# Kernel tuning notes

Measured on AMD Instinct MI355X. Metric: run time of the kernel, lower is better.

The kernel has to match this reference:

```python
import jax, jax.numpy as jnp
import numpy as np

CH = 16      # channel_n
HID = 128    # hidden_n


def _max_pool3(a):
    # a: [B,1,H,W]; 3x3 max pool, stride 1, padding 1 (matches F.max_pool2d)
    return jax.lax.reduce_window(
        a, -jnp.inf, jax.lax.max,
        window_dimensions=(1, 1, 3, 3),
        window_strides=(1, 1, 1, 1),
        padding=((0, 0), (0, 0), (1, 1), (1, 1)))


def _living_mask(x):
    return _max_pool3(x[:, 3:4]) > 0.1


def _nca_step(x, perceive_w, w1, b1, w2, key):
    pre_life = _living_mask(x)                                  # [B,1,H,W] bool
    # depthwise sobel conv, identical weight layout/groups as torch Conv2d(groups=CH)
    p = jax.lax.conv_general_dilated(
        x, perceive_w, window_strides=(1, 1),
        padding=((1, 1), (1, 1)),
        dimension_numbers=('NCHW', 'OIHW', 'NCHW'),
        feature_group_count=CH)                                  # [B,2*CH,H,W]
    comb = jnp.transpose(jnp.concatenate([x, p], axis=1), (0, 2, 3, 1))  # [B,H,W,3*CH]
    h = jax.nn.relu(comb @ w1 + b1)                              # [B,H,W,HID]
    delta = jnp.transpose(h @ w2, (0, 3, 1, 2))                  # [B,CH,H,W]
    alpha = x[:, 3:4]
    upd = (jax.random.uniform(key, alpha.shape, dtype=x.dtype) < 0.5) & (alpha > 0.1)
    x = x + delta * upd.astype(x.dtype)
    life = pre_life & _living_mask(x)
    return x * life.astype(x.dtype)


def setup_inputs() -> dict:
    key = jax.random.key(0)
    kx, k1, k2 = jax.random.split(key, 3)
    B, H, W = 2, 128, 128
    x = jax.random.uniform(kx, (B, CH, H, W), dtype=jnp.float32)
    sobel_x = jnp.array([[-1., 0., 1.], [-2., 0., 2.], [-1., 0., 1.]], dtype=jnp.float32)
    sobel_y = jnp.array([[-1., -2., -1.], [0., 0., 0.], [1., 2., 1.]], dtype=jnp.float32)
    wx = jnp.tile(sobel_x[None, None], (CH, 1, 1, 1))
    wy = jnp.tile(sobel_y[None, None], (CH, 1, 1, 1))
    perceive_w = jnp.concatenate([wx, wy], axis=0)               # [2*CH,1,3,3]
    w1 = jax.random.normal(k1, (CH * 3, HID), dtype=jnp.float32) * 0.02
    b1 = jnp.zeros((HID,), dtype=jnp.float32)
    w2 = jax.random.normal(k2, (HID, CH), dtype=jnp.float32) * 0.02
    return {"x": x, "perceive_w": perceive_w, "w1": w1, "b1": b1, "w2": w2, "steps": 64}


def reference(x, perceive_w, w1, b1, w2, steps):
    keys = jax.random.split(jax.random.key(42), steps)

    def body(carry, k):
        return _nca_step(carry, perceive_w, w1, b1, w2, k), None

    x, _ = jax.lax.scan(body, x, keys)
    return x
```

## Files before the change

### kernel.cpp

```cpp
#include <hip/hip_runtime.h>
#include <stdint.h>

#define HH 128
#define WW 128
#define CHN 16
#define NPIX (HH*WW)
#define PLANE (CHN*NPIX)
#define STEPS 64
#define TW 8
#define TH 8

__host__ __device__ __forceinline__ uint32_t rotl32_(uint32_t x, int d) {
  return (x << d) | (x >> (32 - d));
}

__host__ __device__ __forceinline__ void tf2x32(uint32_t k0, uint32_t k1,
                                                uint32_t x0, uint32_t x1,
                                                uint32_t* o0, uint32_t* o1) {
  uint32_t ks0 = k0, ks1 = k1, ks2 = k0 ^ k1 ^ 0x1BD11BDAu;
  x0 += ks0; x1 += ks1;
  x0 += x1; x1 = rotl32_(x1, 13); x1 ^= x0;
  x0 += x1; x1 = rotl32_(x1, 15); x1 ^= x0;
  x0 += x1; x1 = rotl32_(x1, 26); x1 ^= x0;
  x0 += x1; x1 = rotl32_(x1, 6);  x1 ^= x0;
  x0 += ks1; x1 += ks2 + 1u;
  x0 += x1; x1 = rotl32_(x1, 17); x1 ^= x0;
  x0 += x1; x1 = rotl32_(x1, 29); x1 ^= x0;
  x0 += x1; x1 = rotl32_(x1, 16); x1 ^= x0;
  x0 += x1; x1 = rotl32_(x1, 24); x1 ^= x0;
  x0 += ks2; x1 += ks0 + 2u;
  x0 += x1; x1 = rotl32_(x1, 13); x1 ^= x0;
  x0 += x1; x1 = rotl32_(x1, 15); x1 ^= x0;
  x0 += x1; x1 = rotl32_(x1, 26); x1 ^= x0;
  x0 += x1; x1 = rotl32_(x1, 6);  x1 ^= x0;
  x0 += ks0; x1 += ks1 + 3u;
  x0 += x1; x1 = rotl32_(x1, 17); x1 ^= x0;
  x0 += x1; x1 = rotl32_(x1, 29); x1 ^= x0;
  x0 += x1; x1 = rotl32_(x1, 16); x1 ^= x0;
  x0 += x1; x1 = rotl32_(x1, 24); x1 ^= x0;
  x0 += ks1; x1 += ks2 + 4u;
  x0 += x1; x1 = rotl32_(x1, 13); x1 ^= x0;
  x0 += x1; x1 = rotl32_(x1, 15); x1 ^= x0;
  x0 += x1; x1 = rotl32_(x1, 26); x1 ^= x0;
  x0 += x1; x1 = rotl32_(x1, 6);  x1 ^= x0;
  x0 += ks2; x1 += ks0 + 5u;
  *o0 = x0; *o1 = x1;
}

__global__ void prep_w1t(const float* __restrict__ w1, float* __restrict__ w1t) {
  int i = blockIdx.x * 256 + threadIdx.x;
  if (i < 48 * 128) {
    int j = i / 48, k = i % 48;
    w1t[i] = w1[k * 128 + j];
  }
}

template <int MASKED>
__global__ __launch_bounds__(512, 4) void nca_step(
    const float* __restrict__ xin, const float* __restrict__ plin,
    const float* __restrict__ pw, const float* __restrict__ w1t,
    const float* __restrict__ b1, const float* __restrict__ w2,
    float* __restrict__ xout, float* __restrict__ plout,
    uint32_t k0, uint32_t k1)
{
  __shared__ float xt[CHN][TH + 2][TW + 2];
  __shared__ float Axt[TH + 4][TW + 4];
  __shared__ float Lf[TH + 2][TW + 2];
  __shared__ float combS[64][49];
  __shared__ float dbuf[8][64][17];
  __shared__ float uLDS[64];

  const int tid = threadIdx.x;
  const int blk = blockIdx.x;
  const int b  = blk >> 8;
  const int oh = ((blk >> 4) & 15) * TH;
  const int ow = (blk & 15) * TW;
  const float* xb = xin + (size_t)b * PLANE;

  if (MASKED) {
    const float* ax = xb + 3 * NPIX;
    for (int i = tid; i < (TH + 4) * (TW + 4); i += 512) {
      int r = i / (TW + 4), c = i % (TW + 4);
      int gh = oh + r - 2, gw = ow + c - 2;
      Axt[r][c] = (gh >= 0 && gh < HH && gw >= 0 && gw < WW)
                      ? ax[gh * WW + gw] : 0.f;
    }
  }
  for (int i = tid; i < CHN * (TH + 2) * (TW + 2); i += 512) {
    int c  = i / ((TH + 2) * (TW + 2));
    int r  = (i / (TW + 2)) % (TH + 2);
    int cc = i % (TW + 2);
    int gh = oh + r - 1, gw = ow + cc - 1;
    xt[c][r][cc] = (gh >= 0 && gh < HH && gw >= 0 && gw < WW)
                       ? xb[(c * HH + gh) * WW + gw] : 0.f;
  }
  __syncthreads();

  if (MASKED) {
    const float* pl = plin + b * NPIX;
    for (int i = tid; i < (TH + 2) * (TW + 2); i += 512) {
      int r = i / (TW + 2), c = i % (TW + 2);
      int gh = oh + r - 1, gw = ow + c - 1;
      float life = 0.f;
      if (gh >= 0 && gh < HH && gw >= 0 && gw < WW) {
        float m = Axt[r][c];
        m = fmaxf(m, Axt[r][c + 1]);     m = fmaxf(m, Axt[r][c + 2]);
        m = fmaxf(m, Axt[r + 1][c]);     m = fmaxf(m, Axt[r + 1][c + 1]);
        m = fmaxf(m, Axt[r + 1][c + 2]); m = fmaxf(m, Axt[r + 2][c]);
        m = fmaxf(m, Axt[r + 2][c + 1]); m = fmaxf(m, Axt[r + 2][c + 2]);
        if (m > 0.1f && pl[gh * WW + gw] > 0.5f) life = 1.f;
      }
      Lf[r][c] = life;
    }
    __syncthreads();
    for (int i = tid; i < CHN * (TH + 2) * (TW + 2); i += 512) {
      int c  = i / ((TH + 2) * (TW + 2));
      int rc = i % ((TH + 2) * (TW + 2));
      int r = rc / (TW + 2), cc = rc % (TW + 2);
      xt[c][r][cc] *= Lf[r][cc];
    }
    __syncthreads();
  }

  const int wv   = __builtin_amdgcn_readfirstlane((int)threadIdx.x) >> 6;
  const int lane = tid & 63;
  const int pr = lane >> 3, pc = lane & 7;
  const int gidx = (oh + pr) * WW + (ow + pc);

  {
    const int cA = 2 * wv, cB = 2 * wv + 1;
    float nA[9], nB[9];
    #pragma unroll
    for (int dy = 0; dy < 3; ++dy)
      #pragma unroll
      for (int dx = 0; dx < 3; ++dx) {
        nA[dy * 3 + dx] = xt[cA][pr + dy][pc + dx];
        nB[dy * 3 + dx] = xt[cB][pr + dy][pc + dx];
      }
    float pA0 = 0.f, pA1 = 0.f, pB0 = 0.f, pB1 = 0.f;
    #pragma unroll
    for (int i = 0; i < 9; ++i) {
      pA0 = fmaf(pw[(2 * cA) * 9 + i],     nA[i], pA0);
      pA1 = fmaf(pw[(2 * cA + 1) * 9 + i], nA[i], pA1);
      pB0 = fmaf(pw[(2 * cB) * 9 + i],     nB[i], pB0);
      pB1 = fmaf(pw[(2 * cB + 1) * 9 + i], nB[i], pB1);
    }
    combS[lane][cA] = nA[4];
    combS[lane][cB] = nB[4];
    combS[lane][16 + 2 * cA] = pA0;
    combS[lane][17 + 2 * cA] = pA1;
    combS[lane][16 + 2 * cB] = pB0;
    combS[lane][17 + 2 * cB] = pB1;
    if (wv == 1) {
      float m = nB[0];
      #pragma unroll
      for (int i = 1; i < 9; ++i) m = fmaxf(m, nB[i]);
      plout[b * NPIX + gidx] = (m > 0.1f) ? 1.f : 0.f;
    }
  }
  __syncthreads();

  float comb[48];
  #pragma unroll
  for (int k = 0; k < 48; ++k) comb[k] = combS[lane][k];
  #pragma unroll
  for (int k = 0; k < 48; ++k) asm volatile("" : "+v"(comb[k]));

  if (wv == 0) {
    uint32_t o0, o1;
    tf2x32(k0, k1, 0u, (uint32_t)(b * NPIX + gidx), &o0, &o1);
    const uint32_t bits = o0 ^ o1;
    uLDS[lane] = (((bits >> 31) == 0u) && (comb[3] > 0.1f)) ? 1.f : 0.f;
  }

  const int jbase = wv * 16;
  float delta[16];
  #pragma unroll
  for (int c = 0; c < 16; ++c) delta[c] = 0.f;
  for (int jj = 0; jj < 16; jj += 2) {
    const int j0 = jbase + jj;
    const float* wr0 = w1t + j0 * 48;
    const float* wr1 = wr0 + 48;
    float h0 = b1[j0], h1 = b1[j0 + 1];
    #pragma unroll
    for (int k = 0; k < 48; ++k) {
      h0 = fmaf(comb[k], wr0[k], h0);
      h1 = fmaf(comb[k], wr1[k], h1);
    }
    h0 = fmaxf(h0, 0.f); h1 = fmaxf(h1, 0.f);
    const float* w20 = w2 + j0 * 16;
    #pragma unroll
    for (int c = 0; c < 16; ++c)
      delta[c] = fmaf(h0, w20[c], fmaf(h1, w20[16 + c], delta[c]));
  }

  #pragma unroll
  for (int c = 0; c < 16; ++c) dbuf[wv][lane][c] = delta[c];
  __syncthreads();

  const float u = uLDS[lane];
  float* qb = xout + (size_t)b * PLANE;
  #pragma unroll
  for (int c2 = 0; c2 < 2; ++c2) {
    const int c = 2 * wv + c2;
    float s = dbuf[0][lane][c];
    #pragma unroll
    for (int t = 1; t < 8; ++t) s += dbuf[t][lane][c];
    qb[c * NPIX + gidx] = fmaf(s, u, comb[c]);
  }
}

__global__ __launch_bounds__(256, 2) void nca_fin(
    const float* __restrict__ xl, const float* __restrict__ pl,
    float* __restrict__ out)
{
  __shared__ float Axt[TH + 4][TW + 4];
  const int tid = threadIdx.x;
  const int blk = blockIdx.x;
  const int b  = blk >> 8;
  const int oh = ((blk >> 4) & 15) * TH;
  const int ow = (blk & 15) * TW;
  const float* ax = xl + (size_t)b * PLANE + 3 * NPIX;
  for (int i = tid; i < (TH + 4) * (TW + 4); i += 256) {
    int r = i / (TW + 4), c = i % (TW + 4);
    int gh = oh + r - 2, gw = ow + c - 2;
    Axt[r][c] = (gh >= 0 && gh < HH && gw >= 0 && gw < WW)
                    ? ax[gh * WW + gw] : 0.f;
  }
  __syncthreads();
  const int wv = tid >> 6, lane = tid & 63;
  const int pr = lane >> 3, pc = lane & 7;
  const int gidx = (oh + pr) * WW + (ow + pc);
  float m = Axt[pr + 1][pc + 1];
  #pragma unroll
  for (int dy = 0; dy < 3; ++dy)
    #pragma unroll
    for (int dx = 0; dx < 3; ++dx)
      m = fmaxf(m, Axt[pr + 1 + dy][pc + 1 + dx]);
  const float lf = (m > 0.1f && pl[b * NPIX + gidx] > 0.5f) ? 1.f : 0.f;
  const float* qb = xl + (size_t)b * PLANE;
  float* ob = out + (size_t)b * PLANE;
  #pragma unroll
  for (int c2 = 0; c2 < 4; ++c2) {
    const int c = wv * 4 + c2;
    ob[c * NPIX + gidx] = qb[c * NPIX + gidx] * lf;
  }
}

extern "C" void kernel_launch(void* const* d_in, const int* in_sizes, int n_in,
                              void* d_out, int out_size, void* d_ws, size_t ws_size,
                              hipStream_t stream) {
  (void)in_sizes; (void)n_in; (void)out_size; (void)ws_size;
  const float* x  = (const float*)d_in[0];
  const float* pw = (const float*)d_in[1];
  const float* w1 = (const float*)d_in[2];
  const float* b1 = (const float*)d_in[3];
  const float* w2 = (const float*)d_in[4];

  float* out = (float*)d_out;
  float* ws  = (float*)d_ws;
  float* xb0 = ws;
  float* xb1 = ws + 2 * PLANE;
  float* pb0 = ws + 4 * PLANE;
  float* pb1 = ws + 4 * PLANE + 2 * NPIX;
  float* w1t = ws + 4 * PLANE + 4 * NPIX;

  prep_w1t<<<(48 * 128 + 255) / 256, 256, 0, stream>>>(w1, w1t);

  uint32_t key0[STEPS], key1[STEPS];
  for (uint32_t s = 0; s < STEPS; ++s)
    tf2x32(0u, 42u, 0u, s, &key0[s], &key1[s]);

  float* xbuf[2] = { xb0, xb1 };
  float* pbuf[2] = { pb0, pb1 };
  nca_step<0><<<dim3(512), dim3(512), 0, stream>>>(
      x, nullptr, pw, w1t, b1, w2, xbuf[0], pbuf[0], key0[0], key1[0]);
  for (int s = 1; s < STEPS; ++s) {
    nca_step<1><<<dim3(512), dim3(512), 0, stream>>>(
        xbuf[(s - 1) & 1], pbuf[(s - 1) & 1], pw, w1t, b1, w2,
        xbuf[s & 1], pbuf[s & 1], key0[s], key1[s]);
  }
  const int lf = (STEPS - 1) & 1;
  nca_fin<<<dim3(512), dim3(256), 0, stream>>>(xbuf[lf], pbuf[lf], out);
}
```

Before: 1.252 ms.

## Stage MLP weights in LDS and repartition hidden units across lanes with shuffle reduction

```diff
diff --git a/kernel.cpp b/kernel.cpp
--- a/kernel.cpp
+++ b/kernel.cpp
@@ -9,6 +9,9 @@
 #define STEPS 64
 #define TW 8
 #define TH 8
+#define W1P 52
+#define W2P 20
+#define CBP 52
 
 __host__ __device__ __forceinline__ uint32_t rotl32_(uint32_t x, int d) {
   return (x << d) | (x >> (32 - d));
@@ -66,9 +69,11 @@
   __shared__ float xt[CHN][TH + 2][TW + 2];
   __shared__ float Axt[TH + 4][TW + 4];
   __shared__ float Lf[TH + 2][TW + 2];
-  __shared__ float combS[64][49];
-  __shared__ float dbuf[8][64][17];
+  __shared__ float combS[64][CBP];
   __shared__ float uLDS[64];
+  __shared__ float w1L[128][W1P];
+  __shared__ float w2L[128][W2P];
+  __shared__ float b1L[128];
 
   const int tid = threadIdx.x;
   const int blk = blockIdx.x;
@@ -76,6 +81,18 @@
   const int oh = ((blk >> 4) & 15) * TH;
   const int ow = (blk & 15) * TW;
   const float* xb = xin + (size_t)b * PLANE;
+
+  for (int i = tid; i < (128 * 48) / 4; i += 512) {
+    float4 v = ((const float4*)w1t)[i];
+    int j = (4 * i) / 48, k = (4 * i) % 48;
+    *(float4*)&w1L[j][k] = v;
+  }
+  for (int i = tid; i < (128 * 16) / 4; i += 512) {
+    float4 v = ((const float4*)w2)[i];
+    int j = (4 * i) / 16, c = (4 * i) % 16;
+    *(float4*)&w2L[j][c] = v;
+  }
+  if (tid < 128) b1L[tid] = b1[tid];
 
   if (MASKED) {
     const float* ax = xb + 3 * NPIX;
@@ -124,10 +141,9 @@
 
   const int wv   = __builtin_amdgcn_readfirstlane((int)threadIdx.x) >> 6;
   const int lane = tid & 63;
-  const int pr = lane >> 3, pc = lane & 7;
-  const int gidx = (oh + pr) * WW + (ow + pc);
 
   {
+    const int pr = lane >> 3, pc = lane & 7;
     const int cA = 2 * wv, cB = 2 * wv + 1;
     float nA[9], nB[9];
     #pragma unroll
@@ -155,59 +171,84 @@
       float m = nB[0];
       #pragma unroll
       for (int i = 1; i < 9; ++i) m = fmaxf(m, nB[i]);
-      plout[b * NPIX + gidx] = (m > 0.1f) ? 1.f : 0.f;
+      plout[b * NPIX + (oh + pr) * WW + (ow + pc)] = (m > 0.1f) ? 1.f : 0.f;
     }
   }
   __syncthreads();
 
+  if (wv == 0) {
+    const int gr = (oh + (lane >> 3)) * WW + ow + (lane & 7);
+    uint32_t o0, o1;
+    tf2x32(k0, k1, 0u, (uint32_t)(b * NPIX + gr), &o0, &o1);
+    const uint32_t bits = o0 ^ o1;
+    uLDS[lane] = (((bits >> 31) == 0u) && (combS[lane][3] > 0.1f)) ? 1.f : 0.f;
+  }
+
+  const int pxl = lane & 7, jg = lane >> 3;
+  const int px = wv * 8 + pxl;
+
   float comb[48];
-  #pragma unroll
-  for (int k = 0; k < 48; ++k) comb[k] = combS[lane][k];
+  {
+    const float* cr = &combS[px][0];
+    #pragma unroll
+    for (int q = 0; q < 12; ++q) {
+      float4 v = *(const float4*)(cr + 4 * q);
+      comb[4 * q] = v.x; comb[4 * q + 1] = v.y;
+      comb[4 * q + 2] = v.z; comb[4 * q + 3] = v.w;
+    }
+  }
   #pragma unroll
   for (int k = 0; k < 48; ++k) asm volatile("" : "+v"(comb[k]));
 
-  if (wv == 0) {
-    uint32_t o0, o1;
-    tf2x32(k0, k1, 0u, (uint32_t)(b * NPIX + gidx), &o0, &o1);
-    const uint32_t bits = o0 ^ o1;
-    uLDS[lane] = (((bits >> 31) == 0u) && (comb[3] > 0.1f)) ? 1.f : 0.f;
-  }
-
-  const int jbase = wv * 16;
   float delta[16];
   #pragma unroll
   for (int c = 0; c < 16; ++c) delta[c] = 0.f;
+  #pragma unroll
   for (int jj = 0; jj < 16; jj += 2) {
-    const int j0 = jbase + jj;
-    const float* wr0 = w1t + j0 * 48;
-    const float* wr1 = wr0 + 48;
-    float h0 = b1[j0], h1 = b1[j0 + 1];
-    #pragma unroll
-    for (int k = 0; k < 48; ++k) {
-      h0 = fmaf(comb[k], wr0[k], h0);
-      h1 = fmaf(comb[k], wr1[k], h1);
-    }
-    h0 = fmaxf(h0, 0.f); h1 = fmaxf(h1, 0.f);
-    const float* w20 = w2 + j0 * 16;
-    #pragma unroll
-    for (int c = 0; c < 16; ++c)
-      delta[c] = fmaf(h0, w20[c], fmaf(h1, w20[16 + c], delta[c]));
-  }
-
-  #pragma unroll
-  for (int c = 0; c < 16; ++c) dbuf[wv][lane][c] = delta[c];
+    const int ja = jg + 8 * jj, jb = ja + 8;
+    const float* wa = &w1L[ja][0];
+    const float* wb = &w1L[jb][0];
+    float ha = b1L[ja], hb = b1L[jb];
+    #pragma unroll
+    for (int q = 0; q < 12; ++q) {
+      const float4 a = *(const float4*)(wa + 4 * q);
+      const float4 bq = *(const float4*)(wb + 4 * q);
+      const float c0 = comb[4 * q], c1 = comb[4 * q + 1];
+      const float c2 = comb[4 * q + 2], c3 = comb[4 * q + 3];
+      ha = fmaf(c0, a.x, ha);  ha = fmaf(c1, a.y, ha);
+      ha = fmaf(c2, a.z, ha);  ha = fmaf(c3, a.w, ha);
+      hb = fmaf(c0, bq.x, hb); hb = fmaf(c1, bq.y, hb);
+      hb = fmaf(c2, bq.z, hb); hb = fmaf(c3, bq.w, hb);
+    }
+    ha = fmaxf(ha, 0.f); hb = fmaxf(hb, 0.f);
+    const float* va = &w2L[ja][0];
+    const float* vb = &w2L[jb][0];
+    #pragma unroll
+    for (int q = 0; q < 4; ++q) {
+      const float4 a = *(const float4*)(va + 4 * q);
+      const float4 bq = *(const float4*)(vb + 4 * q);
+      delta[4 * q]     = fmaf(ha, a.x, fmaf(hb, bq.x, delta[4 * q]));
+      delta[4 * q + 1] = fmaf(ha, a.y, fmaf(hb, bq.y, delta[4 * q + 1]));
+      delta[4 * q + 2] = fmaf(ha, a.z, fmaf(hb, bq.z, delta[4 * q + 2]));
+      delta[4 * q + 3] = fmaf(ha, a.w, fmaf(hb, bq.w, delta[4 * q + 3]));
+    }
+  }
+
+  #pragma unroll
+  for (int c = 0; c < 16; ++c) delta[c] += __shfl_xor(delta[c], 8, 64);
+  #pragma unroll
+  for (int c = 0; c < 16; ++c) delta[c] += __shfl_xor(delta[c], 16, 64);
+  #pragma unroll
+  for (int c = 0; c < 16; ++c) delta[c] += __shfl_xor(delta[c], 32, 64);
+
   __syncthreads();
 
-  const float u = uLDS[lane];
+  const float u = uLDS[px];
+  const int gidx = (oh + wv) * WW + (ow + pxl);
   float* qb = xout + (size_t)b * PLANE;
-  #pragma unroll
-  for (int c2 = 0; c2 < 2; ++c2) {
-    const int c = 2 * wv + c2;
-    float s = dbuf[0][lane][c];
-    #pragma unroll
-    for (int t = 1; t < 8; ++t) s += dbuf[t][lane][c];
-    qb[c * NPIX + gidx] = fmaf(s, u, comb[c]);
-  }
+  const int c0 = 2 * jg;
+  qb[c0 * NPIX + gidx]       = fmaf(delta[c0], u, comb[c0]);
+  qb[(c0 + 1) * NPIX + gidx] = fmaf(delta[c0 + 1], u, comb[c0 + 1]);
 }
 
 __global__ __launch_bounds__(256, 2) void nca_fin(
```

Result: slower. 1.531 ms (+22.2%).

## Load halo tiles via global_load_lds DMA and overlap RNG with loads

Applied to the files above, without the earlier changes.

```diff
diff --git a/kernel.cpp b/kernel.cpp
--- a/kernel.cpp
+++ b/kernel.cpp
@@ -9,6 +9,13 @@
 #define STEPS 64
 #define TW 8
 #define TH 8
+
+#define AS1 __attribute__((address_space(1)))
+#define AS3 __attribute__((address_space(3)))
+
+__device__ __forceinline__ void dma4(const float* g, float* l) {
+  __builtin_amdgcn_global_load_lds((const AS1 float*)g, (AS3 float*)l, 4, 0, 0);
+}
 
 __host__ __device__ __forceinline__ uint32_t rotl32_(uint32_t x, int d) {
   return (x << d) | (x >> (32 - d));
@@ -47,12 +54,14 @@
   *o0 = x0; *o1 = x1;
 }
 
-__global__ void prep_w1t(const float* __restrict__ w1, float* __restrict__ w1t) {
+__global__ void prep_w1t(const float* __restrict__ w1, float* __restrict__ w1t,
+                         float* __restrict__ zpad) {
   int i = blockIdx.x * 256 + threadIdx.x;
   if (i < 48 * 128) {
     int j = i / 48, k = i % 48;
     w1t[i] = w1[k * 128 + j];
   }
+  if (blockIdx.x == 0 && threadIdx.x < 64) zpad[threadIdx.x] = 0.f;
 }
 
 template <int MASKED>
@@ -60,15 +69,17 @@
     const float* __restrict__ xin, const float* __restrict__ plin,
     const float* __restrict__ pw, const float* __restrict__ w1t,
     const float* __restrict__ b1, const float* __restrict__ w2,
+    const float* __restrict__ zpad,
     float* __restrict__ xout, float* __restrict__ plout,
     uint32_t k0, uint32_t k1)
 {
-  __shared__ float xt[CHN][TH + 2][TW + 2];
-  __shared__ float Axt[TH + 4][TW + 4];
-  __shared__ float Lf[TH + 2][TW + 2];
+  __shared__ float xtL[CHN * 100];
+  __shared__ float AxtL[144];
+  __shared__ float plL[100];
+  __shared__ float Lf[100];
   __shared__ float combS[64][49];
+  __shared__ uint32_t uBits[64];
   __shared__ float dbuf[8][64][17];
-  __shared__ float uLDS[64];
 
   const int tid = threadIdx.x;
   const int blk = blockIdx.x;
@@ -79,63 +90,68 @@
 
   if (MASKED) {
     const float* ax = xb + 3 * NPIX;
-    for (int i = tid; i < (TH + 4) * (TW + 4); i += 512) {
-      int r = i / (TW + 4), c = i % (TW + 4);
+    if (tid < 144) {
+      int r = tid / 12, c = tid % 12;
       int gh = oh + r - 2, gw = ow + c - 2;
-      Axt[r][c] = (gh >= 0 && gh < HH && gw >= 0 && gw < WW)
-                      ? ax[gh * WW + gw] : 0.f;
-    }
-  }
-  for (int i = tid; i < CHN * (TH + 2) * (TW + 2); i += 512) {
-    int c  = i / ((TH + 2) * (TW + 2));
-    int r  = (i / (TW + 2)) % (TH + 2);
-    int cc = i % (TW + 2);
+      const float* g = (gh >= 0 && gh < HH && gw >= 0 && gw < WW)
+                           ? &ax[gh * WW + gw] : zpad;
+      dma4(g, &AxtL[tid]);
+    }
+    const float* pl = plin + b * NPIX;
+    if (tid < 100) {
+      int r = tid / 10, c = tid % 10;
+      int gh = oh + r - 1, gw = ow + c - 1;
+      const float* g = (gh >= 0 && gh < HH && gw >= 0 && gw < WW)
+                           ? &pl[gh * WW + gw] : zpad;
+      dma4(g, &plL[tid]);
+    }
+  }
+  for (int i = tid; i < CHN * 100; i += 512) {
+    int c = i / 100, rem = i % 100;
+    int r = rem / 10, cc = rem % 10;
     int gh = oh + r - 1, gw = ow + cc - 1;
-    xt[c][r][cc] = (gh >= 0 && gh < HH && gw >= 0 && gw < WW)
-                       ? xb[(c * HH + gh) * WW + gw] : 0.f;
-  }
-  __syncthreads();
-
-  if (MASKED) {
-    const float* pl = plin + b * NPIX;
-    for (int i = tid; i < (TH + 2) * (TW + 2); i += 512) {
-      int r = i / (TW + 2), c = i % (TW + 2);
-      int gh = oh + r - 1, gw = ow + c - 1;
-      float life = 0.f;
-      if (gh >= 0 && gh < HH && gw >= 0 && gw < WW) {
-        float m = Axt[r][c];
-        m = fmaxf(m, Axt[r][c + 1]);     m = fmaxf(m, Axt[r][c + 2]);
-        m = fmaxf(m, Axt[r + 1][c]);     m = fmaxf(m, Axt[r + 1][c + 1]);
-        m = fmaxf(m, Axt[r + 1][c + 2]); m = fmaxf(m, Axt[r + 2][c]);
-        m = fmaxf(m, Axt[r + 2][c + 1]); m = fmaxf(m, Axt[r + 2][c + 2]);
-        if (m > 0.1f && pl[gh * WW + gw] > 0.5f) life = 1.f;
-      }
-      Lf[r][c] = life;
-    }
-    __syncthreads();
-    for (int i = tid; i < CHN * (TH + 2) * (TW + 2); i += 512) {
-      int c  = i / ((TH + 2) * (TW + 2));
-      int rc = i % ((TH + 2) * (TW + 2));
-      int r = rc / (TW + 2), cc = rc % (TW + 2);
-      xt[c][r][cc] *= Lf[r][cc];
-    }
-    __syncthreads();
+    const float* g = (gh >= 0 && gh < HH && gw >= 0 && gw < WW)
+                         ? &xb[(c * HH + gh) * WW + gw] : zpad;
+    dma4(g, &xtL[i]);
   }
 
   const int wv   = __builtin_amdgcn_readfirstlane((int)threadIdx.x) >> 6;
   const int lane = tid & 63;
-  const int pr = lane >> 3, pc = lane & 7;
-  const int gidx = (oh + pr) * WW + (ow + pc);
+
+  if (wv == 0) {
+    const int gr = (oh + (lane >> 3)) * WW + ow + (lane & 7);
+    uint32_t o0, o1;
+    tf2x32(k0, k1, 0u, (uint32_t)(b * NPIX + gr), &o0, &o1);
+    uBits[lane] = o0 ^ o1;
+  }
+  __syncthreads();
+
+  if (MASKED) {
+    if (tid < 100) {
+      int r = tid / 10, c = tid % 10;
+      float m = AxtL[r * 12 + c];
+      m = fmaxf(m, AxtL[r * 12 + c + 1]);        m = fmaxf(m, AxtL[r * 12 + c + 2]);
+      m = fmaxf(m, AxtL[(r + 1) * 12 + c]);      m = fmaxf(m, AxtL[(r + 1) * 12 + c + 1]);
+      m = fmaxf(m, AxtL[(r + 1) * 12 + c + 2]);  m = fmaxf(m, AxtL[(r + 2) * 12 + c]);
+      m = fmaxf(m, AxtL[(r + 2) * 12 + c + 1]);  m = fmaxf(m, AxtL[(r + 2) * 12 + c + 2]);
+      Lf[tid] = (m > 0.1f && plL[tid] > 0.5f) ? 1.f : 0.f;
+    }
+    __syncthreads();
+    for (int i = tid; i < CHN * 100; i += 512)
+      xtL[i] *= Lf[i % 100];
+    __syncthreads();
+  }
 
   {
+    const int pr = lane >> 3, pc = lane & 7;
     const int cA = 2 * wv, cB = 2 * wv + 1;
     float nA[9], nB[9];
     #pragma unroll
     for (int dy = 0; dy < 3; ++dy)
       #pragma unroll
       for (int dx = 0; dx < 3; ++dx) {
-        nA[dy * 3 + dx] = xt[cA][pr + dy][pc + dx];
-        nB[dy * 3 + dx] = xt[cB][pr + dy][pc + dx];
+        nA[dy * 3 + dx] = xtL[cA * 100 + (pr + dy) * 10 + (pc + dx)];
+        nB[dy * 3 + dx] = xtL[cB * 100 + (pr + dy) * 10 + (pc + dx)];
       }
     float pA0 = 0.f, pA1 = 0.f, pB0 = 0.f, pB1 = 0.f;
     #pragma unroll
@@ -155,25 +171,25 @@
       float m = nB[0];
       #pragma unroll
       for (int i = 1; i < 9; ++i) m = fmaxf(m, nB[i]);
-      plout[b * NPIX + gidx] = (m > 0.1f) ? 1.f : 0.f;
+      plout[b * NPIX + (oh + pr) * WW + (ow + pc)] = (m > 0.1f) ? 1.f : 0.f;
     }
   }
   __syncthreads();
 
+  const int jbase = wv * 16;
   float comb[48];
-  #pragma unroll
-  for (int k = 0; k < 48; ++k) comb[k] = combS[lane][k];
+  {
+    const float* cr = &combS[lane][0];
+    #pragma unroll
+    for (int q = 0; q < 12; ++q) {
+      float4 v = *(const float4*)(cr + 4 * q);
+      comb[4 * q] = v.x; comb[4 * q + 1] = v.y;
+      comb[4 * q + 2] = v.z; comb[4 * q + 3] = v.w;
+    }
+  }
   #pragma unroll
   for (int k = 0; k < 48; ++k) asm volatile("" : "+v"(comb[k]));
 
-  if (wv == 0) {
-    uint32_t o0, o1;
-    tf2x32(k0, k1, 0u, (uint32_t)(b * NPIX + gidx), &o0, &o1);
-    const uint32_t bits = o0 ^ o1;
-    uLDS[lane] = (((bits >> 31) == 0u) && (comb[3] > 0.1f)) ? 1.f : 0.f;
-  }
-
-  const int jbase = wv * 16;
   float delta[16];
   #pragma unroll
   for (int c = 0; c < 16; ++c) delta[c] = 0.f;
@@ -198,7 +214,8 @@
   for (int c = 0; c < 16; ++c) dbuf[wv][lane][c] = delta[c];
   __syncthreads();
 
-  const float u = uLDS[lane];
+  const float u = (((uBits[lane] >> 31) == 0u) && (comb[3] > 0.1f)) ? 1.f : 0.f;
+  const int gidx = (oh + (lane >> 3)) * WW + (ow + (lane & 7));
   float* qb = xout + (size_t)b * PLANE;
   #pragma unroll
   for (int c2 = 0; c2 < 2; ++c2) {
@@ -264,8 +281,9 @@
   float* pb0 = ws + 4 * PLANE;
   float* pb1 = ws + 4 * PLANE + 2 * NPIX;
   float* w1t = ws + 4 * PLANE + 4 * NPIX;
-
-  prep_w1t<<<(48 * 128 + 255) / 256, 256, 0, stream>>>(w1, w1t);
+  float* zpad = w1t + 48 * 128;
+
+  prep_w1t<<<(48 * 128 + 255) / 256, 256, 0, stream>>>(w1, w1t, zpad);
 
   uint32_t key0[STEPS], key1[STEPS];
   for (uint32_t s = 0; s < STEPS; ++s)
@@ -274,10 +292,10 @@
   float* xbuf[2] = { xb0, xb1 };
   float* pbuf[2] = { pb0, pb1 };
   nca_step<0><<<dim3(512), dim3(512), 0, stream>>>(
-      x, nullptr, pw, w1t, b1, w2, xbuf[0], pbuf[0], key0[0], key1[0]);
+      x, nullptr, pw, w1t, b1, w2, zpad, xbuf[0], pbuf[0], key0[0], key1[0]);
   for (int s = 1; s < STEPS; ++s) {
     nca_step<1><<<dim3(512), dim3(512), 0, stream>>>(
-        xbuf[(s - 1) & 1], pbuf[(s - 1) & 1], pw, w1t, b1, w2,
+        xbuf[(s - 1) & 1], pbuf[(s - 1) & 1], pw, w1t, b1, w2, zpad,
         xbuf[s & 1], pbuf[s & 1], key0[s], key1[s]);
   }
   const int lf = (STEPS - 1) & 1;
```

Measured after the change: 1.299 ms. +3.7%, slower.
